# Kernel tuning notes

Hardware: AMD Instinct MI355X
Metric: run time of the kernel (lower is better)

Reference implementation:

```python
import jax, jax.numpy as jnp
import numpy as np

# graph metadata: 3 node types, 4 canonical etypes
NT_SRC = (0, 1, 1, 2)   # src ntype of each relation
NT_DST = (1, 0, 2, 1)   # dst ntype of each relation
GROUPS = {0: (1,), 1: (0, 3), 2: (2,)}  # relations sharing each dst ntype (in dict order)
NEG_SLOPE = 0.2
N_NODES, N_EDGES, IN_DIM = 50000, 200000, 256
HEADS, HID = 8, 32
REL_IN, REL_HID = 64, 32


def _leaky(x):
    return jax.nn.leaky_relu(x, NEG_SLOPE)


def _segment_softmax(e, seg, n):
    # numerically stable softmax over edges grouped by dst node
    m = jax.ops.segment_max(e, seg, num_segments=n)
    ex = jnp.exp(e - m[seg])
    s = jax.ops.segment_sum(ex, seg, num_segments=n)
    return ex / s[seg]


def setup_inputs() -> dict:
    key = jax.random.key(0)
    ks = jax.random.split(key, 12)
    w = 0.05  # xavier-like scale
    feat = jax.random.normal(ks[0], (4, N_NODES, IN_DIM), jnp.float32)
    rel_emb = jax.random.normal(ks[1], (4, REL_IN), jnp.float32)
    node_W = jax.random.normal(ks[2], (3, IN_DIM, HEADS * HID), jnp.float32) * w
    rel_W = jax.random.normal(ks[3], (4, REL_IN, HEADS * 2 * HID), jnp.float32) * w
    res_W = jax.random.normal(ks[4], (3, IN_DIM, HEADS * HID), jnp.float32) * w
    res_b = jnp.zeros((3, HEADS * HID), jnp.float32)
    res_alpha = jax.random.normal(ks[5], (3,), jnp.float32)
    cross_attn = jax.random.normal(ks[6], (4, HEADS, HID), jnp.float32) * w
    prop_W = jax.random.normal(ks[7], (4, REL_IN, HEADS * REL_HID), jnp.float32) * w
    prop_b = jnp.zeros((4, HEADS * REL_HID), jnp.float32)
    src_idx = jax.random.randint(ks[8], (4, N_EDGES), 0, N_NODES, jnp.int32)
    dst_idx = jax.random.randint(ks[9], (4, N_EDGES), 0, N_NODES, jnp.int32)
    return dict(feat=feat, rel_emb=rel_emb, node_W=node_W, rel_W=rel_W,
                res_W=res_W, res_b=res_b, res_alpha=res_alpha,
                cross_attn=cross_attn, prop_W=prop_W, prop_b=prop_b,
                src_idx=src_idx, dst_idx=dst_idx)


def reference(feat, rel_emb, node_W, rel_W, res_W, res_b, res_alpha,
              cross_attn, prop_W, prop_b, src_idx, dst_idx):
    R, N, _ = feat.shape
    H, D = HEADS, HID
    conv_out = []
    for r in range(R):  # fixed small set of relations
        s, d = NT_SRC[r], NT_DST[r]
        # RelationGraphConv (dropout is identity in eval)
        fsrc = (feat[r] @ node_W[s]).reshape(N, H, D)
        fdst = (feat[r] @ node_W[d]).reshape(N, H, D)
        ra = (rel_emb[r] @ rel_W[r]).reshape(H, 2 * D)
        e_dst = (fdst * ra[:, :D]).sum(-1)           # (N, H)
        e_src = (fsrc * ra[:, D:]).sum(-1)           # (N, H)
        e = _leaky(e_src[src_idx[r]] + e_dst[dst_idx[r]])  # (E, H)
        a = _segment_softmax(e, dst_idx[r], N)       # edge softmax per dst node
        msg = fsrc[src_idx[r]] * a[:, :, None]       # (E, H, D)
        out = jax.ops.segment_sum(msg, dst_idx[r], num_segments=N)
        out = jax.nn.relu(out.reshape(N, H * D))
        # residual gate
        alpha = jax.nn.sigmoid(res_alpha[d])
        out = out * alpha + (feat[r] @ res_W[d] + res_b[d]) * (1.0 - alpha)
        conv_out.append(out)
    # RelationCrossing over relations sharing the dst ntype
    node_out = []
    for r in range(R):
        group = GROUPS[NT_DST[r]]
        if len(group) == 1:
            node_out.append(conv_out[group[0]])
        else:
            stacked = jnp.stack([conv_out[g] for g in group], 0).reshape(len(group), N, H, D)
            att = _leaky((stacked * cross_attn[r]).sum(-1, keepdims=True))  # (Rg, N, H, 1)
            att = jax.nn.softmax(att, axis=0)
            node_out.append((stacked * att).sum(0).reshape(N, H * D))
    node_out = jnp.stack(node_out, 0)                # (4, N, H*D)
    # relation embedding propagation
    rel_out = jnp.einsum('ri,rio->ro', rel_emb, prop_W) + prop_b  # (4, H*rel_hid)
    return node_out, rel_out
```

## Files before the change

### kernel.cpp

```cpp
#include <hip/hip_runtime.h>
#include <hip/hip_bf16.h>
#include <stdint.h>

typedef unsigned int u32;
typedef unsigned short u16;
typedef short short8 __attribute__((ext_vector_type(8)));
typedef float f32x4 __attribute__((ext_vector_type(4)));
typedef unsigned short u16x4 __attribute__((ext_vector_type(4)));
typedef __attribute__((address_space(1))) const u32 gu32;
typedef __attribute__((address_space(3))) u32 lu32;

#define NN 50000
#define NE 200000
#define WCT 576

__device__ __forceinline__ float leaky(float x){ return x >= 0.f ? x : 0.2f*x; }
__device__ __forceinline__ float bf2f(u16 u){ return __uint_as_float(((u32)u)<<16); }
__device__ __forceinline__ u16 f2bf(float f){
    u32 u = __float_as_uint(f);
    u32 r = (u + 0x7fffu + ((u>>16)&1u)) >> 16;
    return (u16)r;
}
__device__ __forceinline__ u32 pack_bf2(float a, float b){
    return __builtin_amdgcn_perm(__float_as_uint(b), __float_as_uint(a), 0x07060302u);
}
__device__ __forceinline__ int nt_src(int r){ return (r==0)?0:((r==3)?2:1); }
__device__ __forceinline__ int nt_dst(int r){ return (r==1)?0:((r==2)?2:1); }

__global__ void k_ra(const float* __restrict__ rel_emb, const float* __restrict__ rel_W,
                     float* __restrict__ ra){
    int r = blockIdx.x;
    for (int j = threadIdx.x; j < 512; j += blockDim.x){
        float acc = 0.f;
        for (int i = 0; i < 64; i++) acc += rel_emb[r*64+i] * rel_W[(r*64+i)*512 + j];
        ra[r*512 + j] = acc;
    }
}

__global__ void k_wcat(const float* __restrict__ node_W, const float* __restrict__ res_W,
                       const float* __restrict__ ra, u16* __restrict__ WcatS){
    int g = blockIdx.x*blockDim.x + threadIdx.x;
    if (g >= 4*WCT*256) return;
    int r = g/147456; int rem = g%147456;
    int s9 = rem/8192; int rem2 = rem%8192;
    int kc = rem2/256; int rem3 = rem2%256;
    int nrow = rem3>>3; int off = rem3&7;
    int n = s9*32 + nrow;
    int k = kc*8 + off;
    int s = nt_src(r), d = nt_dst(r);
    float v;
    if (n < 256) v = node_W[(s*256+k)*256 + n];
    else if (n < 512) v = res_W[(d*256+k)*256 + (n-256)];
    else if (n < 520){
        int h = n-512; float a = 0.f;
        for (int dd = 0; dd < 32; dd++) a += node_W[(s*256+k)*256 + h*32+dd] * ra[r*512 + h*64+32+dd];
        v = a;
    } else if (n < 528){
        int h = n-520; float a = 0.f;
        for (int dd = 0; dd < 32; dd++) a += node_W[(d*256+k)*256 + h*32+dd] * ra[r*512 + h*64+dd];
        v = a;
    } else v = 0.f;
    WcatS[g] = f2bf(v);
}

__launch_bounds__(512, 6)
__global__ void k_gemm(const float* __restrict__ feat, const u16* __restrict__ WcatS,
                       const float* __restrict__ res_b,
                       u16* __restrict__ fsrc, u16* __restrict__ resb,
                       float* __restrict__ e_comb){
    __shared__ uint4 lsB[2048];
    const short8* lsB8 = (const short8*)lsB;

    int r = blockIdx.y;
    int row0 = blockIdx.x*128;
    const float* A = feat + (size_t)r*NN*256;
    const u16*   W = WcatS + (size_t)r*18*8192;

    int t = threadIdx.x;
    int w = t>>6, l = t&63;
    int wm = w*16;
    int li = l & 15, lg = l >> 4;

    short8 afr[8];
    {
        int grow = row0 + wm + li; if (grow > NN-1) grow = NN-1;
        const float* ap = A + (size_t)grow*256 + lg*8;
        #pragma unroll
        for (int kk = 0; kk < 8; kk++){
            f32x4 x = __builtin_nontemporal_load((const f32x4*)(ap + kk*32));
            f32x4 y = __builtin_nontemporal_load((const f32x4*)(ap + kk*32 + 4));
            short8 f;
            ((u32*)&f)[0] = pack_bf2(x.x, x.y);
            ((u32*)&f)[1] = pack_bf2(x.z, x.w);
            ((u32*)&f)[2] = pack_bf2(y.x, y.y);
            ((u32*)&f)[3] = pack_bf2(y.z, y.w);
            afr[kk] = f;
        }
    }

    #pragma unroll
    for (int i = 0; i < 2; i++){
        int chunk = i*512 + t;
        __builtin_amdgcn_global_load_lds((gu32*)(W + (size_t)chunk*8),
                                         (lu32*)((char*)lsB + chunk*16), 16, 0, 0);
    }
    __syncthreads();

    int d = nt_dst(r);
    int orow = t>>2, oq = t&3;
    int ogrow = row0 + orow;
    size_t onidx = (size_t)r*NN + ogrow;

    for (int s = 0; s < 17; s++){
        int cur = s & 1;
        if (s < 16){
            const u16* tb = W + (size_t)(s+1)*8192;
            char* lb = (char*)lsB + (cur^1)*16384;
            #pragma unroll
            for (int i = 0; i < 2; i++){
                int chunk = i*512 + t;
                __builtin_amdgcn_global_load_lds((gu32*)(tb + (size_t)chunk*8),
                                                 (lu32*)(lb + chunk*16), 16, 0, 0);
            }
        }
        f32x4 acc[2] = {};
        #pragma unroll
        for (int kk = 0; kk < 8; kk++){
            short8 b0 = lsB8[cur*1024 + (kk*4+lg)*32 + li];
            short8 b1 = lsB8[cur*1024 + (kk*4+lg)*32 + 16 + li];
            acc[0] = __builtin_amdgcn_mfma_f32_16x16x32_bf16(afr[kk], b0, acc[0], 0,0,0);
            acc[1] = __builtin_amdgcn_mfma_f32_16x16x32_bf16(afr[kk], b1, acc[1], 0,0,0);
        }
        if (s < 16){
            float bias[2] = {0.f, 0.f};
            if (s >= 8){
                bias[0] = res_b[d*256 + (s-8)*32 + li];
                bias[1] = res_b[d*256 + (s-8)*32 + 16 + li];
            }
            __syncthreads();
            u16* cst = (u16*)(lsB + (size_t)cur*1024);
            #pragma unroll
            for (int nt = 0; nt < 2; nt++)
                #pragma unroll
                for (int qq = 0; qq < 4; qq++)
                    cst[(wm + lg*4 + qq)*36 + nt*16 + li] = f2bf(acc[nt][qq] + bias[nt]);
            __syncthreads();
            if (ogrow < NN){
                u16* dst = (s < 8) ? (fsrc + onidx*256 + s*32) : (resb + onidx*256 + (s-8)*32);
                *(uint4*)(dst + oq*8) = *(const uint4*)(cst + orow*36 + oq*8);
            }
            __syncthreads();
        } else {
            #pragma unroll
            for (int qq = 0; qq < 4; qq++){
                int row = row0 + wm + lg*4 + qq;
                if (row < NN)
                    e_comb[((size_t)r*NN + row)*16 + li] = acc[0][qq];
            }
        }
    }
}


__global__ void k_count(const int* __restrict__ dst_idx, u32* __restrict__ cnt){
    int r = blockIdx.y; int e = blockIdx.x*256 + threadIdx.x;
    if (e >= NE) return;
    atomicAdd(&cnt[r*NN + dst_idx[r*NE+e]], 1u);
}

__global__ void k_scan1(const u32* __restrict__ cnt, u32* __restrict__ bsum){
    int r = blockIdx.y, b = blockIdx.x;
    int i = b*256 + threadIdx.x;
    u32 v = (i < NN) ? cnt[r*NN+i] : 0u;
    #pragma unroll
    for (int off = 1; off < 64; off <<= 1) v += __shfl_xor(v, off, 64);
    __shared__ u32 wsum[4];
    int lane = threadIdx.x & 63, w = threadIdx.x >> 6;
    if (lane == 0) wsum[w] = v;
    __syncthreads();
    if (threadIdx.x == 0) bsum[r*256 + b] = wsum[0]+wsum[1]+wsum[2]+wsum[3];
}

__device__ __forceinline__ u32 block_scan_incl(u32 v){
    __shared__ u32 wsum[4];
    int lane = threadIdx.x & 63, w = threadIdx.x >> 6;
    #pragma unroll
    for (int off = 1; off < 64; off <<= 1){
        u32 t = __shfl_up(v, off, 64);
        if (lane >= off) v += t;
    }
    if (lane == 63) wsum[w] = v;
    __syncthreads();
    u32 add = 0;
    #pragma unroll
    for (int k = 0; k < 4; k++) if (k < w) add += wsum[k];
    return v + add;
}

__global__ void k_scan2(u32* __restrict__ bsum){
    int r = blockIdx.x;
    u32 v = bsum[r*256 + threadIdx.x];
    u32 incl = block_scan_incl(v);
    bsum[r*256 + threadIdx.x] = incl - v;
}

__global__ void k_scan3(const u32* __restrict__ cnt, const u32* __restrict__ bsum,
                        u32* __restrict__ row_ptr){
    int r = blockIdx.y, b = blockIdx.x;
    int i = b*256 + threadIdx.x;
    u32 v = (i < NN) ? cnt[r*NN+i] : 0u;
    u32 incl = block_scan_incl(v);
    if (i < NN) row_ptr[r*(NN+1) + i + 1] = bsum[r*256 + b] + incl;
    if (b == 0 && threadIdx.x == 0) row_ptr[r*(NN+1)] = 0u;
}

__global__ void k_scatter(const int* __restrict__ src_idx, const int* __restrict__ dst_idx,
                          const float* __restrict__ e_comb,
                          const u32* __restrict__ row_ptr, u32* __restrict__ cnt2,
                          u32* __restrict__ src_pack, float* __restrict__ e_pack){
    int r = blockIdx.y; int e = blockIdx.x*256 + threadIdx.x;
    if (e >= NE) return;
    int s = src_idx[r*NE+e], d = dst_idx[r*NE+e];
    u32 pos = row_ptr[r*(NN+1)+d] + atomicAdd(&cnt2[r*NN+d], 1u);
    src_pack[r*NE + pos] = (u32)s;
    const f32x4* es = (const f32x4*)(e_comb + (size_t)(r*NN+s)*16);
    const f32x4* ed = (const f32x4*)(e_comb + (size_t)(r*NN+d)*16 + 8);
    f32x4 s0 = es[0], s1 = es[1], d0 = ed[0], d1 = ed[1];
    f32x4 w0, w1;
    w0.x = __expf(leaky(s0.x+d0.x)); w0.y = __expf(leaky(s0.y+d0.y));
    w0.z = __expf(leaky(s0.z+d0.z)); w0.w = __expf(leaky(s0.w+d0.w));
    w1.x = __expf(leaky(s1.x+d1.x)); w1.y = __expf(leaky(s1.y+d1.y));
    w1.z = __expf(leaky(s1.z+d1.z)); w1.w = __expf(leaky(s1.w+d1.w));
    f32x4* ep = (f32x4*)(e_pack + ((size_t)(r*NE)+pos)*8);
    ep[0] = w0; ep[1] = w1;
}

__device__ __forceinline__ void agg_core(int n, int r, int l, int h,
                                         const u32* __restrict__ row_ptr,
                                         const u32* __restrict__ src_pack,
                                         const float* __restrict__ e_pack,
                                         const u16* __restrict__ fsrc,
                                         const u16* __restrict__ resb,
                                         const float* __restrict__ res_alpha,
                                         float& c0, float& c1, float& c2, float& c3){
    u32 p0 = row_ptr[r*(NN+1)+n];
    u32 p1 = row_ptr[r*(NN+1)+n+1];
    int deg = (int)(p1 - p0);

    float s = 0.f;
    float a0=0.f, a1=0.f, a2=0.f, a3=0.f;
    const size_t ebase = (size_t)r*NE + p0;
    const u16* fbase = fsrc + (size_t)r*NN*256;
    for (int base = 0; base < deg; base += 64){
        int rem = deg - base; if (rem > 64) rem = 64;
        u32 my_src = 0;
        if (l < rem) my_src = src_pack[ebase + base + l];
        int i = 0;
        for (; i+4 <= rem; i += 4){
            u32 s0 = __shfl(my_src, i, 64);
            u32 s1 = __shfl(my_src, i+1, 64);
            u32 s2 = __shfl(my_src, i+2, 64);
            u32 s3 = __shfl(my_src, i+3, 64);
            float ex0 = e_pack[(ebase + base + i)*8 + h];
            float ex1 = e_pack[(ebase + base + i + 1)*8 + h];
            float ex2 = e_pack[(ebase + base + i + 2)*8 + h];
            float ex3 = e_pack[(ebase + base + i + 3)*8 + h];
            ushort4 f0 = *(const ushort4*)(fbase + (size_t)s0*256 + l*4);
            ushort4 f1 = *(const ushort4*)(fbase + (size_t)s1*256 + l*4);
            ushort4 f2 = *(const ushort4*)(fbase + (size_t)s2*256 + l*4);
            ushort4 f3 = *(const ushort4*)(fbase + (size_t)s3*256 + l*4);
            s += ex0 + ex1 + ex2 + ex3;
            a0 += bf2f(f0.x)*ex0 + bf2f(f1.x)*ex1 + bf2f(f2.x)*ex2 + bf2f(f3.x)*ex3;
            a1 += bf2f(f0.y)*ex0 + bf2f(f1.y)*ex1 + bf2f(f2.y)*ex2 + bf2f(f3.y)*ex3;
            a2 += bf2f(f0.z)*ex0 + bf2f(f1.z)*ex1 + bf2f(f2.z)*ex2 + bf2f(f3.z)*ex3;
            a3 += bf2f(f0.w)*ex0 + bf2f(f1.w)*ex1 + bf2f(f2.w)*ex2 + bf2f(f3.w)*ex3;
        }
        for (; i < rem; i++){
            u32 s0 = __shfl(my_src, i, 64);
            float ex0 = e_pack[(ebase + base + i)*8 + h];
            ushort4 f0 = *(const ushort4*)(fbase + (size_t)s0*256 + l*4);
            s += ex0;
            a0 += bf2f(f0.x)*ex0; a1 += bf2f(f0.y)*ex0; a2 += bf2f(f0.z)*ex0; a3 += bf2f(f0.w)*ex0;
        }
    }
    float inv_sh = (deg > 0) ? 1.0f / s : 0.f;

    int d = nt_dst(r);
    float alpha = 1.f/(1.f + __expf(-res_alpha[d]));
    float beta = 1.f - alpha;
    u16x4 rv = __builtin_nontemporal_load((const u16x4*)(resb + ((size_t)r*NN+n)*256 + l*4));
    c0 = fmaxf(a0*inv_sh,0.f)*alpha + bf2f(rv.x)*beta;
    c1 = fmaxf(a1*inv_sh,0.f)*alpha + bf2f(rv.y)*beta;
    c2 = fmaxf(a2*inv_sh,0.f)*alpha + bf2f(rv.z)*beta;
    c3 = fmaxf(a3*inv_sh,0.f)*alpha + bf2f(rv.w)*beta;
}

__launch_bounds__(128)
__global__ void k_agg12(const u32* __restrict__ row_ptr, const u32* __restrict__ src_pack,
                        const float* __restrict__ e_pack, const u16* __restrict__ fsrc,
                        const u16* __restrict__ resb, const float* __restrict__ res_alpha,
                        float* __restrict__ out){
    int n = blockIdx.x;
    int r = 1 + (threadIdx.x >> 6);
    int l = threadIdx.x & 63;
    int h = l >> 3;
    float c0, c1, c2, c3;
    agg_core(n, r, l, h, row_ptr, src_pack, e_pack, fsrc, resb, res_alpha, c0, c1, c2, c3);
    f32x4 o = {c0, c1, c2, c3};
    __builtin_nontemporal_store(o, (f32x4*)(out + ((size_t)r*NN+n)*256 + l*4));
}

__launch_bounds__(128)
__global__ void k_aggx03(const u32* __restrict__ row_ptr, const u32* __restrict__ src_pack,
                         const float* __restrict__ e_pack, const u16* __restrict__ fsrc,
                         const u16* __restrict__ resb, const float* __restrict__ res_alpha,
                         const float* __restrict__ cross_attn, float* __restrict__ out){
    __shared__ float cbuf[2][256];
    __shared__ float dots[4][8];

    int n = blockIdx.x;
    int w = threadIdx.x >> 6;
    int r = w ? 3 : 0;
    int l = threadIdx.x & 63;
    int h = l >> 3;
    float c0, c1, c2, c3;
    agg_core(n, r, l, h, row_ptr, src_pack, e_pack, fsrc, resb, res_alpha, c0, c1, c2, c3);

    int slot = w;
    cbuf[slot][l*4+0] = c0; cbuf[slot][l*4+1] = c1;
    cbuf[slot][l*4+2] = c2; cbuf[slot][l*4+3] = c3;
    const float* ca0 = cross_attn;
    const float* ca3 = cross_attn + 3*256;
    float d0 = c0*ca0[l*4+0] + c1*ca0[l*4+1] + c2*ca0[l*4+2] + c3*ca0[l*4+3];
    float d3 = c0*ca3[l*4+0] + c1*ca3[l*4+1] + c2*ca3[l*4+2] + c3*ca3[l*4+3];
    #pragma unroll
    for (int msk = 1; msk < 8; msk <<= 1){
        d0 += __shfl_xor(d0, msk, 64);
        d3 += __shfl_xor(d3, msk, 64);
    }
    if ((l & 7) == 0){
        dots[slot*2+0][h] = d0;
        dots[slot*2+1][h] = d3;
    }
    __syncthreads();
    float g0 = (r == 0) ? dots[0][h] : dots[1][h];
    float g3 = (r == 0) ? dots[2][h] : dots[3][h];
    g0 = leaky(g0); g3 = leaky(g3);
    float mm = fmaxf(g0, g3);
    float w0 = __expf(g0-mm), w3 = __expf(g3-mm);
    float inv = 1.f/(w0+w3);
    w0 *= inv; w3 *= inv;
    f32x4 o;
    o.x = w0*cbuf[0][l*4+0] + w3*cbuf[1][l*4+0];
    o.y = w0*cbuf[0][l*4+1] + w3*cbuf[1][l*4+1];
    o.z = w0*cbuf[0][l*4+2] + w3*cbuf[1][l*4+2];
    o.w = w0*cbuf[0][l*4+3] + w3*cbuf[1][l*4+3];
    __builtin_nontemporal_store(o, (f32x4*)(out + ((size_t)r*NN+n)*256 + l*4));
}

__global__ void k_relout(const float* __restrict__ rel_emb, const float* __restrict__ prop_W,
                         const float* __restrict__ prop_b, float* __restrict__ out){
    int r = blockIdx.x; int o = threadIdx.x;
    float acc = prop_b[r*256 + o];
    for (int i = 0; i < 64; i++) acc += rel_emb[r*64+i] * prop_W[(r*64+i)*256 + o];
    out[(size_t)4*NN*256 + r*256 + o] = acc;
}

extern "C" void kernel_launch(void* const* d_in, const int* in_sizes, int n_in,
                              void* d_out, int out_size, void* d_ws, size_t ws_size,
                              hipStream_t stream){
    const float* feat      = (const float*)d_in[0];
    const float* rel_emb   = (const float*)d_in[1];
    const float* node_W    = (const float*)d_in[2];
    const float* rel_W     = (const float*)d_in[3];
    const float* res_W     = (const float*)d_in[4];
    const float* res_b     = (const float*)d_in[5];
    const float* res_alpha = (const float*)d_in[6];
    const float* cross_attn= (const float*)d_in[7];
    const float* prop_W    = (const float*)d_in[8];
    const float* prop_b    = (const float*)d_in[9];
    const int* src_idx     = (const int*)d_in[10];
    const int* dst_idx     = (const int*)d_in[11];
    float* out = (float*)d_out;

    char* ws = (char*)d_ws;
    u32*   cnt     = (u32*)  (ws);
    u32*   cnt2    = (u32*)  (ws + 800000);
    u32*   bsum    = (u32*)  (ws + 1600000);
    u32*   row_ptr = (u32*)  (ws + 1604096);
    float* ra      = (float*)(ws + 2404112);
    u16*   WcatS   = (u16*)  (ws + 2412304);
    float* e_comb  = (float*)(ws + 3591952);
    u32*   src_pack= (u32*)  (ws + 16391952);
    float* e_pack  = (float*)(ws + 19591952);
    u16*   fsrc    = (u16*)  (ws + 45191952);
    u16*   resb    = (u16*)  (ws + 147591952);

    hipMemsetAsync(cnt, 0, 1604096, stream);

    k_ra<<<4, 256, 0, stream>>>(rel_emb, rel_W, ra);
    k_wcat<<<(4*WCT*256)/256, 256, 0, stream>>>(node_W, res_W, ra, WcatS);
    dim3 gg((NN+127)/128, 4);
    k_gemm<<<gg, 512, 0, stream>>>(feat, WcatS, res_b, fsrc, resb, e_comb);

    dim3 geg((NE+255)/256, 4);
    k_count<<<geg, 256, 0, stream>>>(dst_idx, cnt);
    dim3 gsc((NN+255)/256, 4);
    k_scan1<<<gsc, 256, 0, stream>>>(cnt, bsum);
    k_scan2<<<4, 256, 0, stream>>>(bsum);
    k_scan3<<<gsc, 256, 0, stream>>>(cnt, bsum, row_ptr);
    k_scatter<<<geg, 256, 0, stream>>>(src_idx, dst_idx, e_comb, row_ptr, cnt2,
                                       src_pack, e_pack);
    k_agg12<<<NN, 128, 0, stream>>>(row_ptr, src_pack, e_pack, fsrc, resb,
                                    res_alpha, out);
    k_aggx03<<<NN, 128, 0, stream>>>(row_ptr, src_pack, e_pack, fsrc, resb,
                                     res_alpha, cross_attn, out);
    k_relout<<<4, 256, 0, stream>>>(rel_emb, prop_W, prop_b, out);
}
```

Before: 405.4 us.

## Widen GEMM N-tile to 64 columns with split-K LDS stages and deferred stores

The weight layout is reorganised so each of the 9 GEMM passes covers 64 output columns, split into two K halves loaded into separate LDS buffers. This halves the number of passes and barriers and gives 4 MFMA accumulators per wave for more ILP. The staged output tile moves to its own LDS buffer so its global store can be deferred and overlapped with the next pass's loads. A-matrix loads switch from nontemporal to regular loads. The cost is extra LDS for the staging buffer (about 17 KB), which may reduce occupancy.

```diff
diff --git a/kernel.cpp b/kernel.cpp
--- a/kernel.cpp
+++ b/kernel.cpp
@@ -42,11 +42,11 @@
     int g = blockIdx.x*blockDim.x + threadIdx.x;
     if (g >= 4*WCT*256) return;
     int r = g/147456; int rem = g%147456;
-    int s9 = rem/8192; int rem2 = rem%8192;
-    int kc = rem2/256; int rem3 = rem2%256;
+    int s18 = rem/8192; int rem2 = rem%8192;
+    int kc = rem2/512; int rem3 = rem2%512;
     int nrow = rem3>>3; int off = rem3&7;
-    int n = s9*32 + nrow;
-    int k = kc*8 + off;
+    int n = (s18>>1)*64 + nrow;
+    int k = (s18&1)*128 + kc*8 + off;
     int s = nt_src(r), d = nt_dst(r);
     float v;
     if (n < 256) v = node_W[(s*256+k)*256 + n];
@@ -69,6 +69,7 @@
                        u16* __restrict__ fsrc, u16* __restrict__ resb,
                        float* __restrict__ e_comb){
     __shared__ uint4 lsB[2048];
+    __shared__ u16  cst[128*68];
     const short8* lsB8 = (const short8*)lsB;
 
     int r = blockIdx.y;
@@ -87,8 +88,8 @@
         const float* ap = A + (size_t)grow*256 + lg*8;
         #pragma unroll
         for (int kk = 0; kk < 8; kk++){
-            f32x4 x = __builtin_nontemporal_load((const f32x4*)(ap + kk*32));
-            f32x4 y = __builtin_nontemporal_load((const f32x4*)(ap + kk*32 + 4));
+            f32x4 x = *(const f32x4*)(ap + kk*32);
+            f32x4 y = *(const f32x4*)(ap + kk*32 + 4);
             short8 f;
             ((u32*)&f)[0] = pack_bf2(x.x, x.y);
             ((u32*)&f)[1] = pack_bf2(x.z, x.w);
@@ -111,44 +112,71 @@
     int ogrow = row0 + orow;
     size_t onidx = (size_t)r*NN + ogrow;
 
-    for (int s = 0; s < 17; s++){
-        int cur = s & 1;
-        if (s < 16){
-            const u16* tb = W + (size_t)(s+1)*8192;
-            char* lb = (char*)lsB + (cur^1)*16384;
+    for (int p = 0; p < 9; p++){
+        f32x4 acc[4] = {};
+        {
+            const u16* tb = W + (size_t)(2*p+1)*8192;
             #pragma unroll
             for (int i = 0; i < 2; i++){
                 int chunk = i*512 + t;
                 __builtin_amdgcn_global_load_lds((gu32*)(tb + (size_t)chunk*8),
-                                                 (lu32*)(lb + chunk*16), 16, 0, 0);
+                                                 (lu32*)((char*)lsB + 16384 + chunk*16), 16, 0, 0);
             }
         }
-        f32x4 acc[2] = {};
+        if (p >= 1 && ogrow < NN){
+            int sp = p-1;
+            u16* dst = (sp < 4) ? (fsrc + onidx*256 + sp*64) : (resb + onidx*256 + (sp-4)*64);
+            const uint4* src = (const uint4*)(cst + orow*68 + oq*16);
+            uint4* dq = (uint4*)(dst + oq*16);
+            dq[0] = src[0];
+            dq[1] = src[1];
+        }
         #pragma unroll
-        for (int kk = 0; kk < 8; kk++){
-            short8 b0 = lsB8[cur*1024 + (kk*4+lg)*32 + li];
-            short8 b1 = lsB8[cur*1024 + (kk*4+lg)*32 + 16 + li];
-            acc[0] = __builtin_amdgcn_mfma_f32_16x16x32_bf16(afr[kk], b0, acc[0], 0,0,0);
-            acc[1] = __builtin_amdgcn_mfma_f32_16x16x32_bf16(afr[kk], b1, acc[1], 0,0,0);
-        }
-        if (s < 16){
-            float bias[2] = {0.f, 0.f};
-            if (s >= 8){
-                bias[0] = res_b[d*256 + (s-8)*32 + li];
-                bias[1] = res_b[d*256 + (s-8)*32 + 16 + li];
+        for (int sl = 0; sl < 4; sl++){
+            int kc4 = sl*4 + lg;
+            short8 b0 = lsB8[kc4*64 + li];
+            short8 b1 = lsB8[kc4*64 + 16 + li];
+            short8 b2 = lsB8[kc4*64 + 32 + li];
+            short8 b3 = lsB8[kc4*64 + 48 + li];
+            acc[0] = __builtin_amdgcn_mfma_f32_16x16x32_bf16(afr[sl], b0, acc[0], 0,0,0);
+            acc[1] = __builtin_amdgcn_mfma_f32_16x16x32_bf16(afr[sl], b1, acc[1], 0,0,0);
+            acc[2] = __builtin_amdgcn_mfma_f32_16x16x32_bf16(afr[sl], b2, acc[2], 0,0,0);
+            acc[3] = __builtin_amdgcn_mfma_f32_16x16x32_bf16(afr[sl], b3, acc[3], 0,0,0);
+        }
+        __syncthreads();
+        if (p < 8){
+            const u16* tb = W + (size_t)(2*p+2)*8192;
+            #pragma unroll
+            for (int i = 0; i < 2; i++){
+                int chunk = i*512 + t;
+                __builtin_amdgcn_global_load_lds((gu32*)(tb + (size_t)chunk*8),
+                                                 (lu32*)((char*)lsB + chunk*16), 16, 0, 0);
             }
-            __syncthreads();
-            u16* cst = (u16*)(lsB + (size_t)cur*1024);
+        }
+        #pragma unroll
+        for (int sl = 0; sl < 4; sl++){
+            int kc4 = sl*4 + lg;
+            short8 b0 = lsB8[1024 + kc4*64 + li];
+            short8 b1 = lsB8[1024 + kc4*64 + 16 + li];
+            short8 b2 = lsB8[1024 + kc4*64 + 32 + li];
+            short8 b3 = lsB8[1024 + kc4*64 + 48 + li];
+            acc[0] = __builtin_amdgcn_mfma_f32_16x16x32_bf16(afr[4+sl], b0, acc[0], 0,0,0);
+            acc[1] = __builtin_amdgcn_mfma_f32_16x16x32_bf16(afr[4+sl], b1, acc[1], 0,0,0);
+            acc[2] = __builtin_amdgcn_mfma_f32_16x16x32_bf16(afr[4+sl], b2, acc[2], 0,0,0);
+            acc[3] = __builtin_amdgcn_mfma_f32_16x16x32_bf16(afr[4+sl], b3, acc[3], 0,0,0);
+        }
+        if (p < 8){
+            float bias[4] = {0.f, 0.f, 0.f, 0.f};
+            if (p >= 4){
+                #pragma unroll
+                for (int cf = 0; cf < 4; cf++)
+                    bias[cf] = res_b[d*256 + (p-4)*64 + cf*16 + li];
+            }
             #pragma unroll
-            for (int nt = 0; nt < 2; nt++)
+            for (int cf = 0; cf < 4; cf++)
                 #pragma unroll
                 for (int qq = 0; qq < 4; qq++)
-                    cst[(wm + lg*4 + qq)*36 + nt*16 + li] = f2bf(acc[nt][qq] + bias[nt]);
-            __syncthreads();
-            if (ogrow < NN){
-                u16* dst = (s < 8) ? (fsrc + onidx*256 + s*32) : (resb + onidx*256 + (s-8)*32);
-                *(uint4*)(dst + oq*8) = *(const uint4*)(cst + orow*36 + oq*8);
-            }
+                    cst[(wm + lg*4 + qq)*68 + cf*16 + li] = f2bf(acc[cf][qq] + bias[cf]);
             __syncthreads();
         } else {
             #pragma unroll
@@ -158,6 +186,13 @@
                     e_comb[((size_t)r*NN + row)*16 + li] = acc[0][qq];
             }
         }
+    }
+    if (ogrow < NN){
+        u16* dst = resb + onidx*256 + 3*64;
+        const uint4* src = (const uint4*)(cst + orow*68 + oq*16);
+        uint4* dq = (uint4*)(dst + oq*16);
+        dq[0] = src[0];
+        dq[1] = src[1];
     }
 }
 
```

Measured after the change: 417.5 us. 1.03x slower.

## Split each wave into two half-waves gathering alternate edges with 16-byte loads

Applied to the files above, without the earlier changes.

The aggregation core now has each half of a 64-lane wave process alternate edges, with each lane loading 8 bf16 features (16 bytes) instead of 4. Partial sums are combined across halves with a cross-half shuffle, and the output column mapping and cross-attention reduction are remapped to match. This is meant to raise memory-level parallelism and load width on the irregular gather and to drop the per-chunk broadcast shuffles. In exchange each lane holds more accumulators and needs an extra reduction step, and the loop is no longer unrolled by four.

```diff
diff --git a/kernel.cpp b/kernel.cpp
--- a/kernel.cpp
+++ b/kernel.cpp
@@ -7,6 +7,7 @@
 typedef short short8 __attribute__((ext_vector_type(8)));
 typedef float f32x4 __attribute__((ext_vector_type(4)));
 typedef unsigned short u16x4 __attribute__((ext_vector_type(4)));
+typedef unsigned short u16x8 __attribute__((ext_vector_type(8)));
 typedef __attribute__((address_space(1))) const u32 gu32;
 typedef __attribute__((address_space(3))) u32 lu32;
 
@@ -235,7 +236,7 @@
     ep[0] = w0; ep[1] = w1;
 }
 
-__device__ __forceinline__ void agg_core(int n, int r, int l, int h,
+__device__ __forceinline__ void agg_core(int n, int r, int l,
                                          const u32* __restrict__ row_ptr,
                                          const u32* __restrict__ src_pack,
                                          const float* __restrict__ e_pack,
@@ -243,56 +244,42 @@
                                          const u16* __restrict__ resb,
                                          const float* __restrict__ res_alpha,
                                          float& c0, float& c1, float& c2, float& c3){
+    int half = l >> 5, q = l & 31, h = q >> 2;
     u32 p0 = row_ptr[r*(NN+1)+n];
     u32 p1 = row_ptr[r*(NN+1)+n+1];
     int deg = (int)(p1 - p0);
-
-    float s = 0.f;
-    float a0=0.f, a1=0.f, a2=0.f, a3=0.f;
     const size_t ebase = (size_t)r*NE + p0;
     const u16* fbase = fsrc + (size_t)r*NN*256;
-    for (int base = 0; base < deg; base += 64){
-        int rem = deg - base; if (rem > 64) rem = 64;
-        u32 my_src = 0;
-        if (l < rem) my_src = src_pack[ebase + base + l];
-        int i = 0;
-        for (; i+4 <= rem; i += 4){
-            u32 s0 = __shfl(my_src, i, 64);
-            u32 s1 = __shfl(my_src, i+1, 64);
-            u32 s2 = __shfl(my_src, i+2, 64);
-            u32 s3 = __shfl(my_src, i+3, 64);
-            float ex0 = e_pack[(ebase + base + i)*8 + h];
-            float ex1 = e_pack[(ebase + base + i + 1)*8 + h];
-            float ex2 = e_pack[(ebase + base + i + 2)*8 + h];
-            float ex3 = e_pack[(ebase + base + i + 3)*8 + h];
-            ushort4 f0 = *(const ushort4*)(fbase + (size_t)s0*256 + l*4);
-            ushort4 f1 = *(const ushort4*)(fbase + (size_t)s1*256 + l*4);
-            ushort4 f2 = *(const ushort4*)(fbase + (size_t)s2*256 + l*4);
-            ushort4 f3 = *(const ushort4*)(fbase + (size_t)s3*256 + l*4);
-            s += ex0 + ex1 + ex2 + ex3;
-            a0 += bf2f(f0.x)*ex0 + bf2f(f1.x)*ex1 + bf2f(f2.x)*ex2 + bf2f(f3.x)*ex3;
-            a1 += bf2f(f0.y)*ex0 + bf2f(f1.y)*ex1 + bf2f(f2.y)*ex2 + bf2f(f3.y)*ex3;
-            a2 += bf2f(f0.z)*ex0 + bf2f(f1.z)*ex1 + bf2f(f2.z)*ex2 + bf2f(f3.z)*ex3;
-            a3 += bf2f(f0.w)*ex0 + bf2f(f1.w)*ex1 + bf2f(f2.w)*ex2 + bf2f(f3.w)*ex3;
+
+    float s = 0.f;
+    float a[8] = {0.f,0.f,0.f,0.f,0.f,0.f,0.f,0.f};
+    for (int i = 0; i < deg; i += 2){
+        int e = i + half;
+        u32 src = 0; float ex = 0.f;
+        if (e < deg){
+            src = src_pack[ebase + e];
+            ex  = e_pack[(ebase + e)*8 + h];
         }
-        for (; i < rem; i++){
-            u32 s0 = __shfl(my_src, i, 64);
-            float ex0 = e_pack[(ebase + base + i)*8 + h];
-            ushort4 f0 = *(const ushort4*)(fbase + (size_t)s0*256 + l*4);
-            s += ex0;
-            a0 += bf2f(f0.x)*ex0; a1 += bf2f(f0.y)*ex0; a2 += bf2f(f0.z)*ex0; a3 += bf2f(f0.w)*ex0;
-        }
-    }
-    float inv_sh = (deg > 0) ? 1.0f / s : 0.f;
+        u16x8 f = *(const u16x8*)(fbase + (size_t)src*256 + q*8);
+        s += ex;
+        #pragma unroll
+        for (int j = 0; j < 8; j++) a[j] += bf2f(f[j])*ex;
+    }
+    s += __shfl_xor(s, 32, 64);
+    #pragma unroll
+    for (int j = 0; j < 8; j++) a[j] += __shfl_xor(a[j], 32, 64);
+    float inv = (deg > 0) ? 1.0f / s : 0.f;
 
     int d = nt_dst(r);
     float alpha = 1.f/(1.f + __expf(-res_alpha[d]));
     float beta = 1.f - alpha;
-    u16x4 rv = __builtin_nontemporal_load((const u16x4*)(resb + ((size_t)r*NN+n)*256 + l*4));
-    c0 = fmaxf(a0*inv_sh,0.f)*alpha + bf2f(rv.x)*beta;
-    c1 = fmaxf(a1*inv_sh,0.f)*alpha + bf2f(rv.y)*beta;
-    c2 = fmaxf(a2*inv_sh,0.f)*alpha + bf2f(rv.z)*beta;
-    c3 = fmaxf(a3*inv_sh,0.f)*alpha + bf2f(rv.w)*beta;
+    int cc = q*8 + half*4;
+    u16x4 rv = __builtin_nontemporal_load((const u16x4*)(resb + ((size_t)r*NN+n)*256 + cc));
+    int j0 = half*4;
+    c0 = fmaxf(a[j0+0]*inv,0.f)*alpha + bf2f(rv.x)*beta;
+    c1 = fmaxf(a[j0+1]*inv,0.f)*alpha + bf2f(rv.y)*beta;
+    c2 = fmaxf(a[j0+2]*inv,0.f)*alpha + bf2f(rv.z)*beta;
+    c3 = fmaxf(a[j0+3]*inv,0.f)*alpha + bf2f(rv.w)*beta;
 }
 
 __launch_bounds__(128)
@@ -303,11 +290,11 @@
     int n = blockIdx.x;
     int r = 1 + (threadIdx.x >> 6);
     int l = threadIdx.x & 63;
-    int h = l >> 3;
     float c0, c1, c2, c3;
-    agg_core(n, r, l, h, row_ptr, src_pack, e_pack, fsrc, resb, res_alpha, c0, c1, c2, c3);
+    agg_core(n, r, l, row_ptr, src_pack, e_pack, fsrc, resb, res_alpha, c0, c1, c2, c3);
+    int cc = (l&31)*8 + (l>>5)*4;
     f32x4 o = {c0, c1, c2, c3};
-    __builtin_nontemporal_store(o, (f32x4*)(out + ((size_t)r*NN+n)*256 + l*4));
+    __builtin_nontemporal_store(o, (f32x4*)(out + ((size_t)r*NN+n)*256 + cc));
 }
 
 __launch_bounds__(128)
@@ -322,23 +309,22 @@
     int w = threadIdx.x >> 6;
     int r = w ? 3 : 0;
     int l = threadIdx.x & 63;
-    int h = l >> 3;
+    int half = l >> 5, q = l & 31, h = q >> 2;
+    int cc = q*8 + half*4;
     float c0, c1, c2, c3;
-    agg_core(n, r, l, h, row_ptr, src_pack, e_pack, fsrc, resb, res_alpha, c0, c1, c2, c3);
+    agg_core(n, r, l, row_ptr, src_pack, e_pack, fsrc, resb, res_alpha, c0, c1, c2, c3);
 
     int slot = w;
-    cbuf[slot][l*4+0] = c0; cbuf[slot][l*4+1] = c1;
-    cbuf[slot][l*4+2] = c2; cbuf[slot][l*4+3] = c3;
+    cbuf[slot][cc+0] = c0; cbuf[slot][cc+1] = c1;
+    cbuf[slot][cc+2] = c2; cbuf[slot][cc+3] = c3;
     const float* ca0 = cross_attn;
     const float* ca3 = cross_attn + 3*256;
-    float d0 = c0*ca0[l*4+0] + c1*ca0[l*4+1] + c2*ca0[l*4+2] + c3*ca0[l*4+3];
-    float d3 = c0*ca3[l*4+0] + c1*ca3[l*4+1] + c2*ca3[l*4+2] + c3*ca3[l*4+3];
-    #pragma unroll
-    for (int msk = 1; msk < 8; msk <<= 1){
-        d0 += __shfl_xor(d0, msk, 64);
-        d3 += __shfl_xor(d3, msk, 64);
-    }
-    if ((l & 7) == 0){
+    float d0 = c0*ca0[cc+0] + c1*ca0[cc+1] + c2*ca0[cc+2] + c3*ca0[cc+3];
+    float d3 = c0*ca3[cc+0] + c1*ca3[cc+1] + c2*ca3[cc+2] + c3*ca3[cc+3];
+    d0 += __shfl_xor(d0, 1, 64);  d3 += __shfl_xor(d3, 1, 64);
+    d0 += __shfl_xor(d0, 2, 64);  d3 += __shfl_xor(d3, 2, 64);
+    d0 += __shfl_xor(d0, 32, 64); d3 += __shfl_xor(d3, 32, 64);
+    if ((q & 3) == 0 && half == 0){
         dots[slot*2+0][h] = d0;
         dots[slot*2+1][h] = d3;
     }
@@ -351,11 +337,11 @@
     float inv = 1.f/(w0+w3);
     w0 *= inv; w3 *= inv;
     f32x4 o;
-    o.x = w0*cbuf[0][l*4+0] + w3*cbuf[1][l*4+0];
-    o.y = w0*cbuf[0][l*4+1] + w3*cbuf[1][l*4+1];
-    o.z = w0*cbuf[0][l*4+2] + w3*cbuf[1][l*4+2];
-    o.w = w0*cbuf[0][l*4+3] + w3*cbuf[1][l*4+3];
-    __builtin_nontemporal_store(o, (f32x4*)(out + ((size_t)r*NN+n)*256 + l*4));
+    o.x = w0*cbuf[0][cc+0] + w3*cbuf[1][cc+0];
+    o.y = w0*cbuf[0][cc+1] + w3*cbuf[1][cc+1];
+    o.z = w0*cbuf[0][cc+2] + w3*cbuf[1][cc+2];
+    o.w = w0*cbuf[0][cc+3] + w3*cbuf[1][cc+3];
+    __builtin_nontemporal_store(o, (f32x4*)(out + ((size_t)r*NN+n)*256 + cc));
 }
 
 __global__ void k_relout(const float* __restrict__ rel_emb, const float* __restrict__ prop_W,
```

Measured after the change: 416.0 us. 1.03x slower.
